# Kernel optimization log

Measured on AMD Instinct MI355X. Metric: run time of the kernel, lower is better.

Reference implementation:

```python
import jax, jax.numpy as jnp
import numpy as np

B, S, D = 16, 16, 4096          # batch, q_len, model dim
H, KVH = 32, 8                  # query heads, kv heads (GQA)
HD = D // H                     # head_dim = 128
N_REP = H // KVH                # 4
MAX_B, MAX_S = 16, 4096         # cache dims
ROPE_BASE = 10000.0


def apply_rope(x, start_pos):
    # x: (b, s, h, d); rotate consecutive pairs (x[2i], x[2i+1]) like view_as_complex
    b, s, h, d = x.shape
    theta = 1.0 / (ROPE_BASE ** (jnp.arange(0, d, 2, dtype=jnp.float32) / d))  # (d/2,)
    pos = jnp.arange(start_pos, start_pos + s, dtype=jnp.float32)              # (s,)
    f = pos[:, None] * theta[None, :]                                          # (s, d/2)
    cos = jnp.cos(f)[None, :, None, :]
    sin = jnp.sin(f)[None, :, None, :]
    xp = x.astype(jnp.float32).reshape(b, s, h, d // 2, 2)
    xr, xi = xp[..., 0], xp[..., 1]
    out = jnp.stack([xr * cos - xi * sin, xr * sin + xi * cos], axis=-1)
    return out.reshape(b, s, h, d).astype(x.dtype)


def setup_inputs() -> dict:
    key = jax.random.key(0)
    ks = jax.random.split(key, 8)
    w = 0.02
    return {
        "x": jax.random.normal(ks[0], (B, S, D), jnp.float32),
        "Wq": jax.random.normal(ks[1], (D, H * HD), jnp.float32) * w,
        "Wk": jax.random.normal(ks[2], (D, KVH * HD), jnp.float32) * w,
        "Wv": jax.random.normal(ks[3], (D, KVH * HD), jnp.float32) * w,
        "Wo": jax.random.normal(ks[4], (H * HD, D), jnp.float32) * w,
        # caches hold (simulated) past context keys/values
        "cache_k": jax.random.normal(ks[5], (MAX_B, MAX_S, KVH, HD), jnp.float32),
        "cache_v": jax.random.normal(ks[6], (MAX_B, MAX_S, KVH, HD), jnp.float32),
        "start_pos": MAX_S - S,  # 4080
    }


def reference(x, Wq, Wk, Wv, Wo, cache_k, cache_v, start_pos):
    b, s, _ = x.shape
    kv_len = start_pos + s

    xq = (x @ Wq).reshape(b, s, H, HD)
    xk = (x @ Wk).reshape(b, s, KVH, HD)
    xv = (x @ Wv).reshape(b, s, KVH, HD)

    xq = apply_rope(xq, start_pos)
    xk = apply_rope(xk, start_pos)

    # KV-cache append
    cache_k = cache_k.at[:b, start_pos:start_pos + s].set(xk)
    cache_v = cache_v.at[:b, start_pos:start_pos + s].set(xv)
    keys = cache_k[:b, :kv_len]    # (b, t, kvh, d)
    values = cache_v[:b, :kv_len]  # (b, t, kvh, d)

    # GQA: group query heads per kv head instead of materializing the repeat.
    # repeat_heads maps kv head k -> query heads [k*n_rep, (k+1)*n_rep).
    q = xq.transpose(0, 2, 1, 3).reshape(b, KVH, N_REP, s, HD)

    scores = jnp.einsum('bkrsd,btkd->bkrst', q, keys) / np.sqrt(HD).astype(np.float32)
    attn = jax.nn.softmax(scores.astype(jnp.float32), axis=-1).astype(q.dtype)
    ctx = jnp.einsum('bkrst,btkd->bkrsd', attn, values)  # (b, kvh, n_rep, s, d)

    ctx = ctx.reshape(b, H, s, HD).transpose(0, 2, 1, 3).reshape(b, s, H * HD)
    return ctx @ Wo
```

## Files before the change

### kernel.cpp

```cpp
#include <hip/hip_runtime.h>
#include <hip/hip_bf16.h>

#define D_    4096
#define KVH_  8
#define HD_   128
#define MAXS_ 4096
#define M_    256
#define NCH   8
#define TPC   (MAXS_ / NCH)

using frag_ab = __attribute__((ext_vector_type(8))) short;
using frag_cd = __attribute__((ext_vector_type(4))) float;

__device__ __forceinline__ short bfb(float f) {
  union { float f; unsigned u; } cv; cv.f = f;
  unsigned u = cv.u;
  return (short)((u + 0x7fffu + ((u >> 16) & 1u)) >> 16);
}

#define LDT 72

template<int MODE>
__global__ __launch_bounds__(256) void gemm_bf(
    const short* __restrict__ A_bf, const float* __restrict__ A_f,
    const float* __restrict__ W0, const float* __restrict__ W1,
    const float* __restrict__ W2,
    short* __restrict__ q_bf, short* __restrict__ k_bf, short* __restrict__ v_bf,
    float* __restrict__ Cf, const int* __restrict__ sp)
{
  __shared__ __align__(16) short lds_a[64 * LDT];
  __shared__ __align__(16) short lds_b[64 * LDT];
  int tid = threadIdx.x;
  int wave = tid >> 6, lane = tid & 63, quad = lane >> 4, l16 = lane & 15;
  int m0 = blockIdx.y * 64;
  int n0 = blockIdx.x * 64;

  const float* Wb; int ncols, col;
  if (MODE == 1)       { Wb = W0; ncols = 4096; col = n0; }
  else if (n0 < 4096)  { Wb = W0; ncols = 4096; col = n0; }
  else if (n0 < 5120)  { Wb = W1; ncols = 1024; col = n0 - 4096; }
  else                 { Wb = W2; ncols = 1024; col = n0 - 5120; }

  int tg = tid >> 4, tl = tid & 15;

  const frag_cd fz = {0.f, 0.f, 0.f, 0.f};
  frag_cd acc[4];
#pragma unroll
  for (int i = 0; i < 4; i++) acc[i] = fz;

  float4 rb0, rb1, rb2, rb3;
  float4 ra0, ra1, ra2, ra3;
  frag_ab rabf0, rabf1;

  auto loadB = [&](int kk) {
    const float* base = Wb + (size_t)(kk + tg * 4) * ncols + col + tl * 4;
    rb0 = *(const float4*)(base);
    rb1 = *(const float4*)(base + ncols);
    rb2 = *(const float4*)(base + 2 * ncols);
    rb3 = *(const float4*)(base + 3 * ncols);
  };
  auto loadA = [&](int kk) {
    if (MODE == 0) {
      const float* xb = A_f + (size_t)(m0 + tg) * 4096 + kk + tl * 4;
      ra0 = *(const float4*)(xb);
      ra1 = *(const float4*)(xb + (size_t)16 * 4096);
      ra2 = *(const float4*)(xb + (size_t)32 * 4096);
      ra3 = *(const float4*)(xb + (size_t)48 * 4096);
    } else {
      int m = tid >> 3, k8 = (tid & 7) << 3;
      rabf0 = *(const frag_ab*)(A_bf + (size_t)(m0 + m) * 4096 + kk + k8);
      rabf1 = *(const frag_ab*)(A_bf + (size_t)(m0 + 32 + m) * 4096 + kk + k8);
    }
  };
  auto storeB = [&]() {
    int kb = tg * 4, n4 = tl * 4;
    short4 s;
    s.x = bfb(rb0.x); s.y = bfb(rb1.x); s.z = bfb(rb2.x); s.w = bfb(rb3.x);
    *(short4*)(&lds_b[(n4 + 0) * LDT + kb]) = s;
    s.x = bfb(rb0.y); s.y = bfb(rb1.y); s.z = bfb(rb2.y); s.w = bfb(rb3.y);
    *(short4*)(&lds_b[(n4 + 1) * LDT + kb]) = s;
    s.x = bfb(rb0.z); s.y = bfb(rb1.z); s.z = bfb(rb2.z); s.w = bfb(rb3.z);
    *(short4*)(&lds_b[(n4 + 2) * LDT + kb]) = s;
    s.x = bfb(rb0.w); s.y = bfb(rb1.w); s.z = bfb(rb2.w); s.w = bfb(rb3.w);
    *(short4*)(&lds_b[(n4 + 3) * LDT + kb]) = s;
  };
  auto storeA = [&]() {
    if (MODE == 0) {
      int k4 = tl * 4;
      short4 s;
      s.x = bfb(ra0.x); s.y = bfb(ra0.y); s.z = bfb(ra0.z); s.w = bfb(ra0.w);
      *(short4*)(&lds_a[(0 + tg) * LDT + k4]) = s;
      s.x = bfb(ra1.x); s.y = bfb(ra1.y); s.z = bfb(ra1.z); s.w = bfb(ra1.w);
      *(short4*)(&lds_a[(16 + tg) * LDT + k4]) = s;
      s.x = bfb(ra2.x); s.y = bfb(ra2.y); s.z = bfb(ra2.z); s.w = bfb(ra2.w);
      *(short4*)(&lds_a[(32 + tg) * LDT + k4]) = s;
      s.x = bfb(ra3.x); s.y = bfb(ra3.y); s.z = bfb(ra3.z); s.w = bfb(ra3.w);
      *(short4*)(&lds_a[(48 + tg) * LDT + k4]) = s;
    } else {
      int m = tid >> 3, k8 = (tid & 7) << 3;
      *(frag_ab*)(&lds_a[m * LDT + k8]) = rabf0;
      *(frag_ab*)(&lds_a[(32 + m) * LDT + k8]) = rabf1;
    }
  };

  loadA(0); loadB(0);
  for (int kk = 0; kk < 4096; kk += 64) {
    __syncthreads();
    storeA(); storeB();
    if (kk + 64 < 4096) { loadA(kk + 64); loadB(kk + 64); }
    asm volatile("s_waitcnt lgkmcnt(0)" ::: "memory");
    __builtin_amdgcn_s_barrier();
    __builtin_amdgcn_sched_barrier(0);
#pragma unroll
    for (int k0 = 0; k0 < 64; k0 += 32) {
      frag_ab af = *(const frag_ab*)(&lds_a[(wave * 16 + l16) * LDT + k0 + quad * 8]);
#pragma unroll
      for (int nt = 0; nt < 4; nt++) {
        frag_ab bfr = *(const frag_ab*)(&lds_b[(nt * 16 + l16) * LDT + k0 + quad * 8]);
        acc[nt] = __builtin_amdgcn_mfma_f32_16x16x32_bf16(af, bfr, acc[nt], 0, 0, 0);
      }
    }
  }

  int start_pos = (MODE == 0) ? *sp : 0;
#pragma unroll
  for (int nt = 0; nt < 4; nt++) {
    int n = n0 + nt * 16 + l16;
#pragma unroll
    for (int r = 0; r < 4; r++) {
      int m = m0 + wave * 16 + quad * 4 + r;
      float v = acc[nt][r];
      if (MODE == 1) {
        Cf[(size_t)m * 4096 + n] = v;
      } else {
        float outv = v;
        if (n < 5120) {
          float partner = __shfl_xor(v, 1);
          int hd = n & (HD_ - 1);
          float theta = exp2f(-(float)(hd >> 1) * 0.2076205059304601f);
          float fr = (float)(start_pos + (m & 15)) * theta;
          float sn, cs;
          sincosf(fr, &sn, &cs);
          outv = v * cs + ((n & 1) ? partner * sn : -partner * sn);
        }
        short ob = bfb(outv);
        if (n < 4096)      q_bf[(size_t)m * 4096 + n] = ob;
        else if (n < 5120) k_bf[(size_t)m * 1024 + n - 4096] = ob;
        else               v_bf[(size_t)m * 1024 + n - 5120] = ob;
      }
    }
  }
}

#define KLD 136
#define VLD 72
#define PLD 72

__global__ __launch_bounds__(256, 4) void attn_kernel(
    const short* __restrict__ qb,
    const short* __restrict__ kb,
    const short* __restrict__ vb,
    const float* __restrict__ cache_k,
    const float* __restrict__ cache_v,
    float* __restrict__ part_ctx,
    float* __restrict__ part_m,
    float* __restrict__ part_l,
    const int* __restrict__ sp)
{
  __shared__ __align__(16) short k_s[64 * KLD];
  __shared__ __align__(16) short vT[HD_ * VLD];
  short* p_s = k_s;

  int chunk = blockIdx.x, kvh = blockIdx.y, b = blockIdx.z;
  int tid = threadIdx.x;
  int wave = tid >> 6, lane = tid & 63, quad = lane >> 4, l16 = lane & 15;
  int start_pos = *sp;

  frag_ab qf[4];
  {
    const short* qrow = qb + (size_t)(b * 16 + l16) * D_ + (kvh * 4 + wave) * HD_;
#pragma unroll
    for (int k0 = 0; k0 < 4; k0++)
      qf[k0] = *(const frag_ab*)(qrow + k0 * 32 + quad * 8);
  }

  const frag_cd fz = {0.f, 0.f, 0.f, 0.f};
  frag_cd acc_o[8];
#pragma unroll
  for (int i = 0; i < 8; i++) acc_o[i] = fz;
  float m_i[4], l_i[4];
#pragma unroll
  for (int r = 0; r < 4; r++) { m_i[r] = -1e30f; l_i[r] = 0.f; }

  int rloc = tid >> 5;
  int lane32 = tid & 31;
  int hd4 = lane32 * 4;
  const float scale = 0.08838834764831845f;

  for (int it = 0; it < TPC / 64; it++) {
    int t0 = chunk * TPC + it * 64;
    __syncthreads();
#pragma unroll
    for (int pass = 0; pass < 8; pass++) {
      int row = pass * 8 + rloc;
      int t = t0 + row;
      short4 kq, vq;
      if (t < start_pos) {
        size_t off = (((size_t)b * MAXS_ + t) * KVH_ + kvh) * HD_ + hd4;
        float4 k4 = *(const float4*)(cache_k + off);
        float4 v4 = *(const float4*)(cache_v + off);
        kq.x = bfb(k4.x); kq.y = bfb(k4.y); kq.z = bfb(k4.z); kq.w = bfb(k4.w);
        vq.x = bfb(v4.x); vq.y = bfb(v4.y); vq.z = bfb(v4.z); vq.w = bfb(v4.w);
      } else {
        int s = t - start_pos;
        size_t off = (size_t)(b * 16 + s) * (KVH_ * HD_) + kvh * HD_ + hd4;
        kq = *(const short4*)(kb + off);
        vq = *(const short4*)(vb + off);
      }
      *(short4*)(&k_s[row * KLD + hd4]) = kq;
      int cb = row >> 3, wi = row & 7;
      vT[(hd4 + 0) * VLD + (((cb ^ (((hd4 + 0) >> 3) & 7)) << 3) | wi)] = vq.x;
      vT[(hd4 + 1) * VLD + (((cb ^ (((hd4 + 1) >> 3) & 7)) << 3) | wi)] = vq.y;
      vT[(hd4 + 2) * VLD + (((cb ^ (((hd4 + 2) >> 3) & 7)) << 3) | wi)] = vq.z;
      vT[(hd4 + 3) * VLD + (((cb ^ (((hd4 + 3) >> 3) & 7)) << 3) | wi)] = vq.w;
    }
    __syncthreads();

    frag_cd sc[4];
#pragma unroll
    for (int i = 0; i < 4; i++) sc[i] = fz;
#pragma unroll
    for (int k0 = 0; k0 < HD_; k0 += 32) {
#pragma unroll
      for (int nt = 0; nt < 4; nt++) {
        frag_ab bfm = *(const frag_ab*)(&k_s[(nt * 16 + l16) * KLD + k0 + quad * 8]);
        sc[nt] = __builtin_amdgcn_mfma_f32_16x16x32_bf16(qf[k0 >> 5], bfm, sc[nt], 0, 0, 0);
      }
    }

    float alpha[4];
#pragma unroll
    for (int r = 0; r < 4; r++) {
      float mx = fmaxf(fmaxf(sc[0][r], sc[1][r]), fmaxf(sc[2][r], sc[3][r])) * scale;
#pragma unroll
      for (int off = 1; off < 16; off <<= 1) mx = fmaxf(mx, __shfl_xor(mx, off));
      float mnew = fmaxf(m_i[r], mx);
      alpha[r] = __expf(m_i[r] - mnew);
      m_i[r] = mnew;
      float rsum = 0.f;
#pragma unroll
      for (int nt = 0; nt < 4; nt++) {
        float p = __expf(sc[nt][r] * scale - mnew);
        sc[nt][r] = p;
        rsum += p;
      }
#pragma unroll
      for (int off = 1; off < 16; off <<= 1) rsum += __shfl_xor(rsum, off);
      l_i[r] = l_i[r] * alpha[r] + rsum;
    }
#pragma unroll
    for (int nt = 0; nt < 8; nt++)
#pragma unroll
      for (int r = 0; r < 4; r++) acc_o[nt][r] *= alpha[r];

    __syncthreads();
#pragma unroll
    for (int r = 0; r < 4; r++)
#pragma unroll
      for (int nt = 0; nt < 4; nt++)
        p_s[(wave * 16 + quad * 4 + r) * PLD + nt * 16 + l16] = bfb(sc[nt][r]);

#pragma unroll
    for (int k0 = 0; k0 < 64; k0 += 32) {
      frag_ab af = *(const frag_ab*)(&p_s[(wave * 16 + l16) * PLD + k0 + quad * 8]);
      int tb = (k0 >> 3) + quad;
#pragma unroll
      for (int nt = 0; nt < 8; nt++) {
        int hd = nt * 16 + l16;
        frag_ab bfm = *(const frag_ab*)(&vT[hd * VLD + ((tb ^ ((hd >> 3) & 7)) << 3)]);
        acc_o[nt] = __builtin_amdgcn_mfma_f32_16x16x32_bf16(af, bfm, acc_o[nt], 0, 0, 0);
      }
    }
  }

  int blk = ((b * 8 + kvh) << 3) + chunk;
#pragma unroll
  for (int nt = 0; nt < 8; nt++)
#pragma unroll
    for (int r = 0; r < 4; r++) {
      int qrow = wave * 16 + quad * 4 + r;
      part_ctx[((size_t)blk * 64 + qrow) * HD_ + nt * 16 + l16] = acc_o[nt][r];
    }
  if (l16 == 0) {
#pragma unroll
    for (int r = 0; r < 4; r++) {
      int qrow = wave * 16 + quad * 4 + r;
      part_m[blk * 64 + qrow] = m_i[r];
      part_l[blk * 64 + qrow] = l_i[r];
    }
  }
}

__global__ __launch_bounds__(256) void combine_kernel(
    const float* __restrict__ part_ctx, const float* __restrict__ part_m,
    const float* __restrict__ part_l, short* __restrict__ ctx_bf)
{
  int bk = blockIdx.x;
  int b = bk >> 3, kvh = bk & 7;
  int tid = threadIdx.x;
  __shared__ float w_s[8][64];
  __shared__ float inv_l[64];
  if (tid < 64) {
    float M = -1e30f;
#pragma unroll
    for (int c = 0; c < 8; c++) M = fmaxf(M, part_m[(bk * 8 + c) * 64 + tid]);
    float ls = 0.f;
#pragma unroll
    for (int c = 0; c < 8; c++) {
      float w = __expf(part_m[(bk * 8 + c) * 64 + tid] - M);
      w_s[c][tid] = w;
      ls += part_l[(bk * 8 + c) * 64 + tid] * w;
    }
    inv_l[tid] = 1.f / ls;
  }
  __syncthreads();
  for (int idx = tid; idx < 64 * 128; idx += 256) {
    int qrow = idx >> 7, hd = idx & 127;
    float acc = 0.f;
#pragma unroll
    for (int c = 0; c < 8; c++)
      acc += part_ctx[((size_t)(bk * 8 + c) * 64 + qrow) * HD_ + hd] * w_s[c][qrow];
    float val = acc * inv_l[qrow];
    int r = qrow >> 4, s = qrow & 15;
    ctx_bf[(size_t)(b * 16 + s) * D_ + (kvh * 4 + r) * HD_ + hd] = bfb(val);
  }
}

extern "C" void kernel_launch(void* const* d_in, const int* in_sizes, int n_in,
                              void* d_out, int out_size, void* d_ws, size_t ws_size,
                              hipStream_t stream)
{
  const float* x       = (const float*)d_in[0];
  const float* Wq      = (const float*)d_in[1];
  const float* Wk      = (const float*)d_in[2];
  const float* Wv      = (const float*)d_in[3];
  const float* Wo      = (const float*)d_in[4];
  const float* cache_k = (const float*)d_in[5];
  const float* cache_v = (const float*)d_in[6];
  const int*   sp      = (const int*)d_in[7];

  char* w = (char*)d_ws;
  auto alloc = [&](size_t bytes) { char* p = w; w += (bytes + 255) & ~(size_t)255; return p; };
  short* q_bf   = (short*)alloc((size_t)M_ * 4096 * 2);
  short* k_bf   = (short*)alloc((size_t)M_ * 1024 * 2);
  short* v_bf   = (short*)alloc((size_t)M_ * 1024 * 2);
  short* ctx_bf = (short*)alloc((size_t)M_ * 4096 * 2);
  float* part_ctx = (float*)alloc((size_t)1024 * 64 * 128 * 4);
  float* part_m   = (float*)alloc((size_t)1024 * 64 * 4);
  float* part_l   = (float*)alloc((size_t)1024 * 64 * 4);

  gemm_bf<0><<<dim3(6144 / 64, M_ / 64), 256, 0, stream>>>(
      nullptr, x, Wq, Wk, Wv, q_bf, k_bf, v_bf, nullptr, sp);

  attn_kernel<<<dim3(NCH, 8, 16), 256, 0, stream>>>(
      q_bf, k_bf, v_bf, cache_k, cache_v, part_ctx, part_m, part_l, sp);

  combine_kernel<<<128, 256, 0, stream>>>(part_ctx, part_m, part_l, ctx_bf);

  gemm_bf<1><<<dim3(4096 / 64, M_ / 64), 256, 0, stream>>>(
      ctx_bf, nullptr, Wo, nullptr, nullptr, nullptr, nullptr, nullptr, (float*)d_out, sp);
}
```

Before: 739.0 us.

## Register-prefetch next KV tile during attention compute

Splits the K/V tile load into a global-to-register issue phase and an LDS store phase, and issues loads for the next tile before computing on the current one, so global memory latency overlaps with MFMA work. The barrier before the P write is replaced with a raw LDS waitcnt plus s_barrier, so outstanding global loads are not drained there. Occupancy hint drops from 4 to 3 blocks per CU to make room for the prefetch registers, which lowers latency hiding from other waves.

```diff
diff --git a/kernel.cpp b/kernel.cpp
--- a/kernel.cpp
+++ b/kernel.cpp
@@ -156,7 +156,7 @@
 #define VLD 72
 #define PLD 72
 
-__global__ __launch_bounds__(256, 4) void attn_kernel(
+__global__ __launch_bounds__(256, 3) void attn_kernel(
     const short* __restrict__ qb,
     const short* __restrict__ kb,
     const short* __restrict__ vb,
@@ -197,34 +197,49 @@
   int hd4 = lane32 * 4;
   const float scale = 0.08838834764831845f;
 
-  for (int it = 0; it < TPC / 64; it++) {
-    int t0 = chunk * TPC + it * 64;
-    __syncthreads();
+  short4 kq[8], vq[8];
+
+  auto issue_loads = [&](int it) {
 #pragma unroll
     for (int pass = 0; pass < 8; pass++) {
       int row = pass * 8 + rloc;
-      int t = t0 + row;
-      short4 kq, vq;
+      int t = chunk * TPC + it * 64 + row;
+      short4 k2, v2;
       if (t < start_pos) {
         size_t off = (((size_t)b * MAXS_ + t) * KVH_ + kvh) * HD_ + hd4;
         float4 k4 = *(const float4*)(cache_k + off);
         float4 v4 = *(const float4*)(cache_v + off);
-        kq.x = bfb(k4.x); kq.y = bfb(k4.y); kq.z = bfb(k4.z); kq.w = bfb(k4.w);
-        vq.x = bfb(v4.x); vq.y = bfb(v4.y); vq.z = bfb(v4.z); vq.w = bfb(v4.w);
+        k2.x = bfb(k4.x); k2.y = bfb(k4.y); k2.z = bfb(k4.z); k2.w = bfb(k4.w);
+        v2.x = bfb(v4.x); v2.y = bfb(v4.y); v2.z = bfb(v4.z); v2.w = bfb(v4.w);
       } else {
         int s = t - start_pos;
         size_t off = (size_t)(b * 16 + s) * (KVH_ * HD_) + kvh * HD_ + hd4;
-        kq = *(const short4*)(kb + off);
-        vq = *(const short4*)(vb + off);
-      }
-      *(short4*)(&k_s[row * KLD + hd4]) = kq;
+        k2 = *(const short4*)(kb + off);
+        v2 = *(const short4*)(vb + off);
+      }
+      kq[pass] = k2; vq[pass] = v2;
+    }
+  };
+
+  auto stage_write = [&]() {
+#pragma unroll
+    for (int pass = 0; pass < 8; pass++) {
+      int row = pass * 8 + rloc;
+      *(short4*)(&k_s[row * KLD + hd4]) = kq[pass];
       int cb = row >> 3, wi = row & 7;
-      vT[(hd4 + 0) * VLD + (((cb ^ (((hd4 + 0) >> 3) & 7)) << 3) | wi)] = vq.x;
-      vT[(hd4 + 1) * VLD + (((cb ^ (((hd4 + 1) >> 3) & 7)) << 3) | wi)] = vq.y;
-      vT[(hd4 + 2) * VLD + (((cb ^ (((hd4 + 2) >> 3) & 7)) << 3) | wi)] = vq.z;
-      vT[(hd4 + 3) * VLD + (((cb ^ (((hd4 + 3) >> 3) & 7)) << 3) | wi)] = vq.w;
-    }
+      vT[(hd4 + 0) * VLD + (((cb ^ (((hd4 + 0) >> 3) & 7)) << 3) | wi)] = vq[pass].x;
+      vT[(hd4 + 1) * VLD + (((cb ^ (((hd4 + 1) >> 3) & 7)) << 3) | wi)] = vq[pass].y;
+      vT[(hd4 + 2) * VLD + (((cb ^ (((hd4 + 2) >> 3) & 7)) << 3) | wi)] = vq[pass].z;
+      vT[(hd4 + 3) * VLD + (((cb ^ (((hd4 + 3) >> 3) & 7)) << 3) | wi)] = vq[pass].w;
+    }
+  };
+
+  issue_loads(0);
+  for (int it = 0; it < TPC / 64; it++) {
     __syncthreads();
+    stage_write();
+    __syncthreads();
+    if (it + 1 < TPC / 64) issue_loads(it + 1);
 
     frag_cd sc[4];
 #pragma unroll
@@ -263,7 +278,9 @@
 #pragma unroll
       for (int r = 0; r < 4; r++) acc_o[nt][r] *= alpha[r];
 
-    __syncthreads();
+    asm volatile("s_waitcnt lgkmcnt(0)" ::: "memory");
+    __builtin_amdgcn_s_barrier();
+    __builtin_amdgcn_sched_barrier(0);
 #pragma unroll
     for (int r = 0; r < 4; r++)
 #pragma unroll
```

Result: slower. 794.8 us (+7.6%).
